# Kernel tuning notes

Measured on AMD Instinct MI355X. Metric: run time of the kernel, lower is better.

Reference implementation:

```python
import jax, jax.numpy as jnp
import numpy as np

EPS = 1e-5
ROPE_BASE = 10000.0
N_HEAD = 16


def rms_norm(x, eps=EPS):
    return x * jax.lax.rsqrt(jnp.mean(x * x, axis=-1, keepdims=True) + eps)


def rope(x):
    # x: [B, H, L, D]; non-standard interleaved variant from the source:
    # x_odd = x[..., 1::2], x_even = x[..., ::2]
    # y = interleave(y_odd, y_even)
    B, H, L, D = x.shape
    inv_freq = 1.0 / (ROPE_BASE ** (jnp.arange(0, D, 2, dtype=jnp.float32) / D))
    angles = jnp.arange(L, dtype=jnp.float32)[:, None] * inv_freq[None, :]  # [L, D/2]
    cos, sin = jnp.cos(angles), jnp.sin(angles)
    x_odd = x[..., 1::2].astype(jnp.float32)
    x_even = x[..., ::2].astype(jnp.float32)
    y_odd = x_odd * cos - x_even * sin
    y_even = x_odd * sin + x_even * cos
    y = jnp.stack([y_odd, y_even], axis=-1).reshape(B, H, L, D)
    return y.astype(x.dtype)


def setup_inputs() -> dict:
    key = jax.random.key(0)
    k1, k2, k3 = jax.random.split(key, 3)
    B, L, HID = 2, 2048, 2048
    in_std = 0.5 * HID ** (-0.5)
    bound = (3 ** 0.5) * in_std
    x = jax.random.normal(k1, (B, L, HID), dtype=jnp.float32)
    W_qkv = jax.random.uniform(k2, (3 * HID, HID), minval=-bound, maxval=bound, dtype=jnp.float32)
    # out_proj is zero-initialized in the source; use small random weights so the
    # output (and gradients) are non-trivial for correctness checking.
    W_out = jax.random.uniform(k3, (HID, HID), minval=-bound, maxval=bound, dtype=jnp.float32)
    return {"x": x, "W_qkv": W_qkv, "W_out": W_out}


def reference(x, W_qkv, W_out):
    B, L, HID = x.shape
    D = HID // N_HEAD
    qkv = jnp.einsum('blc,fc->blf', x, W_qkv)  # [B, L, 3*HID]
    q, k, v = jnp.split(qkv, 3, axis=-1)
    def heads(t):
        return t.reshape(B, L, N_HEAD, D).transpose(0, 2, 1, 3)  # [B,H,L,D]
    q, k, v = heads(q), heads(k), heads(v)
    q = rope(rms_norm(q))
    k = rope(rms_norm(k))
    scale = 1.0 / jnp.sqrt(jnp.asarray(D, dtype=jnp.float32))
    scores = jnp.einsum('bhqd,bhkd->bhqk', q, k) * scale
    causal = jnp.tril(jnp.ones((L, L), dtype=bool))
    scores = jnp.where(causal, scores, -jnp.inf)
    attn = jax.nn.softmax(scores, axis=-1)
    out = jnp.einsum('bhqk,bhkd->bhqd', attn, v)
    out = out.transpose(0, 2, 1, 3).reshape(B, L, HID)
    return jnp.einsum('blc,fc->blf', out, W_out)
```

## Files before the change

kernel.cpp:

```cpp
#include <hip/hip_runtime.h>
#include <stdint.h>
#include <math.h>

typedef unsigned short u16;
typedef unsigned int u32;
typedef __attribute__((ext_vector_type(8))) short bf16x8;
typedef __attribute__((ext_vector_type(4))) float f32x4;

#define SEQ 2048
#define HID 2048
#define NH  16
#define DH  128
#define NB  2

typedef __attribute__((address_space(1))) const u32 gu32;
typedef __attribute__((address_space(3))) u32 lu32;

__device__ __forceinline__ u16 f2bf(float f) {
  u32 u = __float_as_uint(f);
  return (u16)((u + 0x7fffu + ((u >> 16) & 1u)) >> 16);
}
__device__ __forceinline__ float bf2f(u16 h) { return __uint_as_float(((u32)h) << 16); }

__device__ __forceinline__ void gload_lds16(const void* g, void* l) {
  __builtin_amdgcn_global_load_lds((gu32*)g, (lu32*)l, 16, 0, 0);
}

__global__ __launch_bounds__(256) void k_cvt3(const float* __restrict__ s0, u16* __restrict__ d0, int n0,
                                              const float* __restrict__ s1, u16* __restrict__ d1, int n1,
                                              const float* __restrict__ s2, u16* __restrict__ d2, int n2) {
  int i = blockIdx.x * 256 + threadIdx.x;
  int stride = gridDim.x * 256;
  int total = n0 + n1 + n2;
  for (; i < total; i += stride) {
    const float* s; u16* d; int k = i;
    if (k < n0) { s = s0; d = d0; }
    else if (k < n0 + n1) { s = s1; d = d1; k -= n0; }
    else { s = s2; d = d2; k -= n0 + n1; }
    float4 v = ((const float4*)s)[k];
    ushort4 o;
    o.x = f2bf(v.x); o.y = f2bf(v.y); o.z = f2bf(v.z); o.w = f2bf(v.w);
    ((ushort4*)d)[k] = o;
  }
}

template<int EPI>
__global__ __launch_bounds__(512, 2)
void k_gemm4(const u16* __restrict__ A, const u16* __restrict__ Bm,
             float* __restrict__ Cf, u16* __restrict__ Qr, u16* __restrict__ Kr, u16* __restrict__ Vr,
             int N, int K, int NX) {
  __shared__ alignas(16) char sA0[16384];
  __shared__ alignas(16) char sA1[16384];
  __shared__ alignas(16) char sB0[32768];
  __shared__ alignas(16) char sB1[32768];
  const int tid = threadIdx.x;
  const int wid = tid >> 6, lane = tid & 63;
  const int l15 = lane & 15, l4 = lane >> 4;
  const int wm = wid >> 2, wn = wid & 3;
  const int nwg = gridDim.x, bid = blockIdx.x;
  const int wg = (bid & 7) * (nwg >> 3) + (bid >> 3);
  const int bx = wg % NX, by = wg / NX;
  const int m0 = by * 128, n0 = bx * 256;
  const char* Ab = (const char*)A;
  const char* Bb = (const char*)Bm;
  const size_t rs = (size_t)K * 2;

  int aoff[4][2], boff[4][2];
  #pragma unroll
  for (int mm = 0; mm < 4; ++mm)
    #pragma unroll
    for (int ks = 0; ks < 2; ++ks) {
      int row = wm * 64 + mm * 16 + l15;
      aoff[mm][ks] = row * 128 + ((ks * 64 + 16 * l4) ^ ((row & 7) << 4));
    }
  #pragma unroll
  for (int nn = 0; nn < 4; ++nn)
    #pragma unroll
    for (int ks = 0; ks < 2; ++ks) {
      int row = wn * 64 + nn * 16 + l15;
      boff[nn][ks] = row * 128 + ((ks * 64 + 16 * l4) ^ ((row & 7) << 4));
    }

  f32x4 acc[4][4];
  #pragma unroll
  for (int i = 0; i < 4; ++i)
    #pragma unroll
    for (int jx = 0; jx < 4; ++jx) acc[i][jx] = (f32x4){0.f, 0.f, 0.f, 0.f};
  bf16x8 areg[4][2], breg[4][2];

  auto STG1 = [&](const char* src, char* dst) {
    int o = tid * 16;
    int row = o >> 7, cb = o & 127;
    gload_lds16(src + (size_t)row * rs + (cb ^ ((row & 7) << 4)), dst + wid * 1024);
  };
  auto STG2 = [&](const char* src, char* dst) {
    #pragma unroll
    for (int jj = 0; jj < 2; ++jj) {
      int o = jj * 8192 + tid * 16;
      int row = o >> 7, cb = o & 127;
      gload_lds16(src + (size_t)row * rs + (cb ^ ((row & 7) << 4)), dst + jj * 8192 + wid * 1024);
    }
  };
  auto RD = [&](const char* sA, const char* sB) {
    #pragma unroll
    for (int mm = 0; mm < 4; ++mm)
      #pragma unroll
      for (int ks = 0; ks < 2; ++ks) areg[mm][ks] = *(const bf16x8*)(sA + aoff[mm][ks]);
    #pragma unroll
    for (int nn = 0; nn < 4; ++nn)
      #pragma unroll
      for (int ks = 0; ks < 2; ++ks) breg[nn][ks] = *(const bf16x8*)(sB + boff[nn][ks]);
  };
  auto MF = [&](int ks) {
    #pragma unroll
    for (int mm = 0; mm < 4; ++mm)
      #pragma unroll
      for (int nn = 0; nn < 4; ++nn)
        acc[mm][nn] = __builtin_amdgcn_mfma_f32_16x16x32_bf16(areg[mm][ks], breg[nn][ks], acc[mm][nn], 0, 0, 0);
  };

  const int NIT = K >> 7;
  STG2(Bb + (size_t)n0 * rs, sB0);
  STG2(Bb + (size_t)(n0 + 128) * rs, sB0 + 16384);
  STG1(Ab + (size_t)m0 * rs, sA0);
  STG1(Ab + (size_t)(m0 + 64) * rs, sA0 + 8192);
  STG2(Bb + (size_t)n0 * rs + 128, sB1);
  STG2(Bb + (size_t)(n0 + 128) * rs + 128, sB1 + 16384);
  STG1(Ab + (size_t)m0 * rs + 128, sA1);
  asm volatile("s_waitcnt vmcnt(5)" ::: "memory");
  __builtin_amdgcn_sched_barrier(0);
  __builtin_amdgcn_s_barrier();

  for (int j = 0; j < NIT; ++j) {
    const size_t k1 = (size_t)(2 * j + 1) * 128;
    const size_t k2 = (size_t)(2 * j + 2) * 128;
    const size_t k3 = (size_t)(2 * j + 3) * 128;
    const bool g2 = (j + 1 < NIT);
    RD(sA0, sB0);
    STG1(Ab + (size_t)(m0 + 64) * rs + k1, sA1 + 8192);
    __builtin_amdgcn_s_barrier();
    asm volatile("s_waitcnt lgkmcnt(0)" ::: "memory");
    __builtin_amdgcn_sched_barrier(0);
    __builtin_amdgcn_s_setprio(1); MF(0); __builtin_amdgcn_s_setprio(0);
    __builtin_amdgcn_s_barrier();
    if (g2) {
      STG2(Bb + (size_t)n0 * rs + k2, sB0);
      STG2(Bb + (size_t)(n0 + 128) * rs + k2, sB0 + 16384);
      STG1(Ab + (size_t)m0 * rs + k2, sA0);
    }
    __builtin_amdgcn_s_barrier();
    __builtin_amdgcn_s_setprio(1); MF(1); __builtin_amdgcn_s_setprio(0);
    if (g2) { asm volatile("s_waitcnt vmcnt(5)" ::: "memory"); }
    else    { asm volatile("s_waitcnt vmcnt(0)" ::: "memory"); }
    __builtin_amdgcn_sched_barrier(0);
    __builtin_amdgcn_s_barrier();
    RD(sA1, sB1);
    if (g2) STG1(Ab + (size_t)(m0 + 64) * rs + k2, sA0 + 8192);
    __builtin_amdgcn_s_barrier();
    asm volatile("s_waitcnt lgkmcnt(0)" ::: "memory");
    __builtin_amdgcn_sched_barrier(0);
    __builtin_amdgcn_s_setprio(1); MF(0); __builtin_amdgcn_s_setprio(0);
    __builtin_amdgcn_s_barrier();
    if (g2) {
      STG2(Bb + (size_t)n0 * rs + k3, sB1);
      STG2(Bb + (size_t)(n0 + 128) * rs + k3, sB1 + 16384);
      STG1(Ab + (size_t)m0 * rs + k3, sA1);
    }
    __builtin_amdgcn_s_barrier();
    __builtin_amdgcn_s_setprio(1); MF(1); __builtin_amdgcn_s_setprio(0);
    if (g2) { asm volatile("s_waitcnt vmcnt(5)" ::: "memory"); }
    else    { asm volatile("s_waitcnt vmcnt(0)" ::: "memory"); }
    __builtin_amdgcn_sched_barrier(0);
    __builtin_amdgcn_s_barrier();
  }

  #pragma unroll
  for (int mi = 0; mi < 4; ++mi) {
    #pragma unroll
    for (int ni = 0; ni < 4; ++ni) {
      #pragma unroll
      for (int jj = 0; jj < 4; ++jj) {
        int gm = m0 + wm * 64 + mi * 16 + l4 * 4 + jj;
        int gn = n0 + wn * 64 + ni * 16 + l15;
        float v = acc[mi][ni][jj];
        if (EPI == 0) {
          int b = gm >> 11, l = gm & 2047;
          int which = gn >> 11, hid = gn & 2047;
          int h = hid >> 7, d = hid & 127;
          u16* dst = (which == 0) ? Qr : ((which == 1) ? Kr : Vr);
          dst[((size_t)(b * NH + h) * SEQ + l) * DH + d] = f2bf(v);
        } else {
          Cf[(size_t)gm * N + gn] = v;
        }
      }
    }
  }
}

__global__ __launch_bounds__(256) void k_vtr(const u16* __restrict__ Vr, u16* __restrict__ Vt) {
  __shared__ u16 tile[64][72];
  const int k0 = blockIdx.x * 64, d0 = blockIdx.y * 64, bh = blockIdx.z;
  const u16* src = Vr + ((size_t)bh << 18);
  u16* dst = Vt + ((size_t)bh << 18);
  const int tid = threadIdx.x;
  #pragma unroll
  for (int it = 0; it < 2; ++it) {
    int e = it * 2048 + tid * 8;
    int r = e >> 6, c = e & 63;
    bf16x8 v = *(const bf16x8*)(src + (size_t)(k0 + r) * DH + d0 + c);
    *(bf16x8*)&tile[r][c] = v;
  }
  __syncthreads();
  #pragma unroll
  for (int it = 0; it < 2; ++it) {
    int e = it * 2048 + tid * 8;
    int rd = e >> 6, ck = e & 63;
    bf16x8 w;
    #pragma unroll
    for (int i = 0; i < 8; ++i) w[i] = (short)tile[ck + i][rd];
    *(bf16x8*)(dst + (size_t)(d0 + rd) * SEQ + k0 + ck) = w;
  }
}

__global__ __launch_bounds__(256) void k_nrope2(u16* __restrict__ Qr, u16* __restrict__ Kr, float mq) {
  u16* T = blockIdx.y ? Kr : Qr;
  const float mul = blockIdx.y ? 1.0f : mq;
  const int r = blockIdx.x * 4 + (threadIdx.x >> 6);
  const int lane = threadIdx.x & 63;
  u16* p = T + ((size_t)r << 7) + lane * 2;
  u32 pr = *(const u32*)p;
  float xe = bf2f((u16)(pr & 0xffffu));
  float xo = bf2f((u16)(pr >> 16));
  float ss = xe * xe + xo * xo;
  #pragma unroll
  for (int off = 1; off < 64; off <<= 1) ss += __shfl_xor(ss, off);
  float rinv = rsqrtf(ss * (1.f / 128.f) + 1e-5f);
  float e = xe * rinv, o = xo * rinv;
  int pos = r & (SEQ - 1);
  float freq = exp2f(-0.20762050593046014f * (float)lane);
  float ang = (float)pos * freq;
  float sn, cs;
  sincosf(ang, &sn, &cs);
  u32 outw = (u32)f2bf((o * cs - e * sn) * mul) | ((u32)f2bf((o * sn + e * cs) * mul) << 16);
  *(u32*)p = outw;
}

__device__ __forceinline__ void smax(f32x4 (&sacc)[4], float& m_, float& se,
                                     f32x4* accO, u32 (&pw)[8],
                                     bool diag, int qpos, int kb, int l15, int l4) {
  if (diag) {
    #pragma unroll
    for (int sj = 0; sj < 4; ++sj)
      #pragma unroll
      for (int j = 0; j < 4; ++j) {
        int kpos = kb + sj * 16 + l4 * 4 + j;
        if (kpos > qpos) sacc[sj][j] = -1e30f;
      }
  }
  float mx = sacc[0][0];
  #pragma unroll
  for (int sj = 0; sj < 4; ++sj)
    #pragma unroll
    for (int j = 0; j < 4; ++j) mx = fmaxf(mx, sacc[sj][j]);
  mx = fmaxf(mx, __shfl_xor(mx, 16));
  mx = fmaxf(mx, __shfl_xor(mx, 32));
  if (!__all(mx <= m_ + 8.f)) {
    float mn = fmaxf(m_, mx);
    float corr = __builtin_exp2f(m_ - mn);
    m_ = mn;
    se *= corr;
    float corr4[4];
    #pragma unroll
    for (int j = 0; j < 4; ++j) corr4[j] = __shfl(corr, l4 * 4 + j);
    #pragma unroll
    for (int db = 0; db < 8; ++db) {
      f32x4 a = accO[db];
      #pragma unroll
      for (int j = 0; j < 4; ++j) a[j] *= corr4[j];
      accO[db] = a;
    }
  }
  float sum = 0.f;
  #pragma unroll
  for (int sj = 0; sj < 4; ++sj)
    #pragma unroll
    for (int jp = 0; jp < 2; ++jp) {
      float p0 = __builtin_exp2f(sacc[sj][jp * 2]     - m_);
      float p1 = __builtin_exp2f(sacc[sj][jp * 2 + 1] - m_);
      pw[sj * 2 + jp] = (u32)f2bf(p0) | ((u32)f2bf(p1) << 16);
      sum += p0 + p1;
    }
  sum += __shfl_xor(sum, 16);
  sum += __shfl_xor(sum, 32);
  se += sum;
}

__device__ __forceinline__ void pwrite(char* sPw, const u32 (&pw)[8], int l15, int l4) {
  const int sw = (l15 & 7) << 4;
  char* base = sPw + l15 * 128;
  #pragma unroll
  for (int sj = 0; sj < 4; ++sj)
    #pragma unroll
    for (int jp = 0; jp < 2; ++jp)
      *(u32*)(base + ((sj * 32 + l4 * 8 + jp * 4) ^ sw)) = pw[sj * 2 + jp];
}

__device__ __forceinline__ void stage_kv(const char* Kp, const char* Vtp, int kb,
                                         char* bK, char* bV, int tid, int wid) {
  #pragma unroll
  for (int it = 0; it < 4; ++it) {
    int o = it * 4096 + tid * 16;
    int row = o >> 8, cb = o & 255;
    int scb = cb ^ ((row & 7) << 4);
    gload_lds16(Kp + (size_t)(kb + row) * 256 + scb, &bK[it * 4096 + wid * 1024]);
  }
  #pragma unroll
  for (int it = 0; it < 4; ++it) {
    int o = it * 4096 + tid * 16;
    int row = o >> 7, cb = o & 127;
    int scb = cb ^ ((row & 7) << 4);
    gload_lds16(Vtp + (size_t)row * (SEQ * 2) + kb * 2 + scb, &bV[it * 4096 + wid * 1024]);
  }
}

__global__ __launch_bounds__(256, 2)
void k_attn(const u16* __restrict__ Q, const u16* __restrict__ Kg,
            const u16* __restrict__ Vt, u16* __restrict__ O) {
  __shared__ alignas(16) char sK0[64 * 256];
  __shared__ alignas(16) char sK1[64 * 256];
  __shared__ alignas(16) char sV0[128 * 128];
  __shared__ alignas(16) char sV1[128 * 128];
  __shared__ alignas(16) char sP[4 * 2048];
  const int tid = threadIdx.x, wid = tid >> 6, lane = tid & 63;
  const int l15 = lane & 15, l4 = lane >> 4;
  const int i = blockIdx.x;
  const int xcd = i & 7, slot = i >> 3;
  const int p = slot & 15;
  const int bh = xcd + 8 * (slot >> 4);
  const int b = bh >> 4, h = bh & 15;
  const int tA = p, tB = 31 - p;
  const u16* Qp = Q + ((size_t)bh << 18);
  const char* Kp = (const char*)(Kg + ((size_t)bh << 18));
  const char* Vtp = (const char*)(Vt + ((size_t)bh << 18));
  const int q0A = tA * 64 + wid * 16;
  const int q0B = tB * 64 + wid * 16;

  bf16x8 aqA[4], aqB[4];
  #pragma unroll
  for (int kk = 0; kk < 4; ++kk) {
    aqA[kk] = *(const bf16x8*)(Qp + (size_t)(q0A + l15) * DH + kk * 32 + 8 * l4);
    aqB[kk] = *(const bf16x8*)(Qp + (size_t)(q0B + l15) * DH + kk * 32 + 8 * l4);
  }

  f32x4 accA[8], accB[8];
  #pragma unroll
  for (int i2 = 0; i2 < 8; ++i2) { accA[i2] = (f32x4){0.f,0.f,0.f,0.f}; accB[i2] = (f32x4){0.f,0.f,0.f,0.f}; }
  float mA = -1e30f, mB = -1e30f, seA = 0.f, seB = 0.f;

  char* sPw = sP + wid * 2048;
  const int psw = (l15 & 7) << 4;
  const int nt = tB + 1;

  stage_kv(Kp, Vtp, 0, sK0, sV0, tid, wid);
  for (int t = 0; t < nt; ++t) {
    char* bK = (t & 1) ? sK1 : sK0;
    char* bV = (t & 1) ? sV1 : sV0;
    if (t + 1 < nt) {
      stage_kv(Kp, Vtp, (t + 1) << 6, (t & 1) ? sK0 : sK1, (t & 1) ? sV0 : sV1, tid, wid);
      asm volatile("s_waitcnt vmcnt(8)" ::: "memory");
    } else {
      asm volatile("s_waitcnt vmcnt(0)" ::: "memory");
    }
    __builtin_amdgcn_sched_barrier(0);
    __builtin_amdgcn_s_barrier();

    const int kb = t << 6;
    if (t <= tA) {
      f32x4 sb[4], sa[4];
      __builtin_amdgcn_s_setprio(1);
      #pragma unroll
      for (int sj = 0; sj < 4; ++sj) {
        sb[sj] = (f32x4){0.f,0.f,0.f,0.f};
        sa[sj] = (f32x4){0.f,0.f,0.f,0.f};
        int row = sj * 16 + l15;
        const char* rK = bK + (row << 8);
        int swr = (row & 7) << 4;
        #pragma unroll
        for (int kk = 0; kk < 4; ++kk) {
          bf16x8 bkv = *(const bf16x8*)(rK + ((kk * 64 + 16 * l4) ^ swr));
          sb[sj] = __builtin_amdgcn_mfma_f32_16x16x32_bf16(bkv, aqB[kk], sb[sj], 0, 0, 0);
          sa[sj] = __builtin_amdgcn_mfma_f32_16x16x32_bf16(bkv, aqA[kk], sa[sj], 0, 0, 0);
        }
      }
      __builtin_amdgcn_s_setprio(0);
      u32 pwB[8], pwA[8];
      smax(sb, mB, seB, accB, pwB, false, 0, kb, l15, l4);
      smax(sa, mA, seA, accA, pwA, t == tA, q0A + l15, kb, l15, l4);
      pwrite(sPw, pwB, l15, l4);
      bf16x8 paB0 = *(const bf16x8*)(sPw + l15 * 128 + ((16 * l4) ^ psw));
      bf16x8 paB1 = *(const bf16x8*)(sPw + l15 * 128 + ((64 + 16 * l4) ^ psw));
      pwrite(sPw, pwA, l15, l4);
      bf16x8 paA0 = *(const bf16x8*)(sPw + l15 * 128 + ((16 * l4) ^ psw));
      bf16x8 paA1 = *(const bf16x8*)(sPw + l15 * 128 + ((64 + 16 * l4) ^ psw));
      __builtin_amdgcn_s_setprio(1);
      #pragma unroll
      for (int db = 0; db < 8; ++db) {
        int row = db * 16 + l15;
        const char* vb = bV + row * 128;
        int swr = (row & 7) << 4;
        bf16x8 b0 = *(const bf16x8*)(vb + ((16 * l4) ^ swr));
        bf16x8 b1 = *(const bf16x8*)(vb + ((64 + 16 * l4) ^ swr));
        accB[db] = __builtin_amdgcn_mfma_f32_16x16x32_bf16(paB0, b0, accB[db], 0, 0, 0);
        accA[db] = __builtin_amdgcn_mfma_f32_16x16x32_bf16(paA0, b0, accA[db], 0, 0, 0);
        accB[db] = __builtin_amdgcn_mfma_f32_16x16x32_bf16(paB1, b1, accB[db], 0, 0, 0);
        accA[db] = __builtin_amdgcn_mfma_f32_16x16x32_bf16(paA1, b1, accA[db], 0, 0, 0);
      }
      __builtin_amdgcn_s_setprio(0);
    } else {
      f32x4 sb[4];
      __builtin_amdgcn_s_setprio(1);
      #pragma unroll
      for (int sj = 0; sj < 4; ++sj) {
        sb[sj] = (f32x4){0.f,0.f,0.f,0.f};
        int row = sj * 16 + l15;
        const char* rK = bK + (row << 8);
        int swr = (row & 7) << 4;
        #pragma unroll
        for (int kk = 0; kk < 4; ++kk) {
          bf16x8 bkv = *(const bf16x8*)(rK + ((kk * 64 + 16 * l4) ^ swr));
          sb[sj] = __builtin_amdgcn_mfma_f32_16x16x32_bf16(bkv, aqB[kk], sb[sj], 0, 0, 0);
        }
      }
      __builtin_amdgcn_s_setprio(0);
      u32 pwB[8];
      smax(sb, mB, seB, accB, pwB, t == tB, q0B + l15, kb, l15, l4);
      pwrite(sPw, pwB, l15, l4);
      bf16x8 paB0 = *(const bf16x8*)(sPw + l15 * 128 + ((16 * l4) ^ psw));
      bf16x8 paB1 = *(const bf16x8*)(sPw + l15 * 128 + ((64 + 16 * l4) ^ psw));
      __builtin_amdgcn_s_setprio(1);
      #pragma unroll
      for (int db = 0; db < 8; ++db) {
        int row = db * 16 + l15;
        const char* vb = bV + row * 128;
        int swr = (row & 7) << 4;
        bf16x8 b0 = *(const bf16x8*)(vb + ((16 * l4) ^ swr));
        bf16x8 b1 = *(const bf16x8*)(vb + ((64 + 16 * l4) ^ swr));
        accB[db] = __builtin_amdgcn_mfma_f32_16x16x32_bf16(paB0, b0, accB[db], 0, 0, 0);
        accB[db] = __builtin_amdgcn_mfma_f32_16x16x32_bf16(paB1, b1, accB[db], 0, 0, 0);
      }
      __builtin_amdgcn_s_setprio(0);
    }

    __builtin_amdgcn_s_barrier();
  }

  float seA4[4], seB4[4];
  #pragma unroll
  for (int j = 0; j < 4; ++j) {
    seA4[j] = __shfl(seA, l4 * 4 + j);
    seB4[j] = __shfl(seB, l4 * 4 + j);
  }
  #pragma unroll
  for (int db = 0; db < 8; ++db) {
    #pragma unroll
    for (int j = 0; j < 4; ++j) {
      int d = db * 16 + l15;
      int qA = q0A + l4 * 4 + j;
      int qB = q0B + l4 * 4 + j;
      O[(size_t)(b * SEQ + qA) * HID + h * DH + d] = f2bf(accA[db][j] / seA4[j]);
      O[(size_t)(b * SEQ + qB) * HID + h * DH + d] = f2bf(accB[db][j] / seB4[j]);
    }
  }
}

extern "C" void kernel_launch(void* const* d_in, const int* in_sizes, int n_in,
                              void* d_out, int out_size, void* d_ws, size_t ws_size,
                              hipStream_t stream) {
  (void)in_sizes; (void)n_in; (void)out_size; (void)ws_size;
  const float* x = (const float*)d_in[0];
  const float* Wqkv = (const float*)d_in[1];
  const float* Wout = (const float*)d_in[2];
  float* out = (float*)d_out;
  char* ws = (char*)d_ws;

  u16* xb  = (u16*)(ws);
  u16* wqb = (u16*)(ws + (size_t)16777216);
  u16* Vt  = wqb;
  u16* wob = (u16*)(ws + (size_t)16777216 + 25165824);
  u16* Qr  = (u16*)(ws + (size_t)50331648);
  u16* Kr  = Qr + (size_t)8388608;
  u16* Vr  = Kr + (size_t)8388608;
  u16* Ob  = xb;

  const float mq = 0.08838834764831845f * 1.4426950408889634f;

  k_cvt3<<<dim3(2048), dim3(256), 0, stream>>>(x, xb, (NB * SEQ * HID) / 4,
                                               Wqkv, wqb, (3 * HID * HID) / 4,
                                               Wout, wob, (HID * HID) / 4);

  k_gemm4<0><<<dim3(768), dim3(512), 0, stream>>>(xb, wqb, nullptr, Qr, Kr, Vr, 3 * HID, HID, 24);

  k_vtr<<<dim3(SEQ / 64, DH / 64, NB * NH), dim3(256), 0, stream>>>(Vr, Vt);
  k_nrope2<<<dim3((NB * NH * SEQ) / 4, 2), dim3(256), 0, stream>>>(Qr, Kr, mq);

  k_attn<<<dim3(512), dim3(256), 0, stream>>>(Qr, Kr, Vt, Ob);

  k_gemm4<1><<<dim3(256), dim3(512), 0, stream>>>(Ob, wob, out, nullptr, nullptr, nullptr, HID, HID, 8);
}
```

Measured before the change: 311.3 us.

## Restructure attention to 256-query blocks and use simple 128x128 QKV GEMM

Attention now launches 256 blocks of 512 threads, each owning a contiguous 256-query slab with eight waves each handling 32 adjacent rows, instead of pairing a short and long 64-row tile to balance causal work. Per-wave activity and diagonal masking flags are computed per KV tile. The QKV projection switches from the double-buffered 512-thread GEMM to a new single-buffered 128x128 GEMM with 1536 blocks. The slab mapping gives blocks unequal causal work (4 to 32 KV tiles), and the new GEMM loses load/compute overlap, so both changes risk poorer utilisation.

```diff
diff --git a/kernel.cpp b/kernel.cpp
--- a/kernel.cpp
+++ b/kernel.cpp
@@ -41,6 +41,95 @@
     ushort4 o;
     o.x = f2bf(v.x); o.y = f2bf(v.y); o.z = f2bf(v.z); o.w = f2bf(v.w);
     ((ushort4*)d)[k] = o;
+  }
+}
+
+template<int EPI>
+__global__ __launch_bounds__(256)
+void k_gemm(const u16* __restrict__ A, const u16* __restrict__ Bm,
+            float* __restrict__ Cf, u16* __restrict__ Qr, u16* __restrict__ Kr, u16* __restrict__ Vr,
+            int N, int K, int NX) {
+  __shared__ alignas(16) char sA[128 * 128];
+  __shared__ alignas(16) char sB[128 * 128];
+  const int tid = threadIdx.x;
+  const int wid = tid >> 6, lane = tid & 63;
+  const int l15 = lane & 15, l4 = lane >> 4;
+  const int nwg = gridDim.x, bid = blockIdx.x;
+  const int wg = (bid & 7) * (nwg >> 3) + (bid >> 3);
+  const int bx = wg % NX, by = wg / NX;
+  const int m0 = by * 128, n0 = bx * 128;
+  const int wr = (wid >> 1) * 64, wc = (wid & 1) * 64;
+
+  f32x4 acc[4][4];
+  #pragma unroll
+  for (int i = 0; i < 4; ++i)
+    #pragma unroll
+    for (int j = 0; j < 4; ++j)
+      acc[i][j] = (f32x4){0.f, 0.f, 0.f, 0.f};
+
+  const int nkt = K >> 6;
+  for (int kt = 0; kt < nkt; ++kt) {
+    const int k0 = kt << 6;
+    __syncthreads();
+    #pragma unroll
+    for (int it = 0; it < 4; ++it) {
+      int o = it * 4096 + tid * 16;
+      int row = o >> 7, cb = o & 127;
+      int scb = cb ^ ((row & 7) << 4);
+      gload_lds16((const char*)A + ((size_t)(m0 + row) * K + k0) * 2 + scb, &sA[it * 4096 + wid * 1024]);
+    }
+    #pragma unroll
+    for (int it = 0; it < 4; ++it) {
+      int o = it * 4096 + tid * 16;
+      int row = o >> 7, cb = o & 127;
+      int scb = cb ^ ((row & 7) << 4);
+      gload_lds16((const char*)Bm + ((size_t)(n0 + row) * K + k0) * 2 + scb, &sB[it * 4096 + wid * 1024]);
+    }
+    __syncthreads();
+    #pragma unroll
+    for (int kk = 0; kk < 2; ++kk) {
+      bf16x8 av[4], bv[4];
+      #pragma unroll
+      for (int mi = 0; mi < 4; ++mi) {
+        int row = wr + mi * 16 + l15;
+        int colb = kk * 64 + 16 * l4;
+        av[mi] = *(const bf16x8*)&sA[row * 128 + (colb ^ ((row & 7) << 4))];
+      }
+      #pragma unroll
+      for (int ni = 0; ni < 4; ++ni) {
+        int row = wc + ni * 16 + l15;
+        int colb = kk * 64 + 16 * l4;
+        bv[ni] = *(const bf16x8*)&sB[row * 128 + (colb ^ ((row & 7) << 4))];
+      }
+      #pragma unroll
+      for (int mi = 0; mi < 4; ++mi)
+        #pragma unroll
+        for (int ni = 0; ni < 4; ++ni)
+          acc[mi][ni] = __builtin_amdgcn_mfma_f32_16x16x32_bf16(av[mi], bv[ni], acc[mi][ni], 0, 0, 0);
+    }
+  }
+
+  #pragma unroll
+  for (int mi = 0; mi < 4; ++mi) {
+    #pragma unroll
+    for (int ni = 0; ni < 4; ++ni) {
+      #pragma unroll
+      for (int j = 0; j < 4; ++j) {
+        int gm = m0 + wr + mi * 16 + l4 * 4 + j;
+        int gn = n0 + wc + ni * 16 + l15;
+        float v = acc[mi][ni][j];
+        if (EPI == 0) {
+          int b = gm >> 11, l = gm & 2047;
+          int which = gn >> 11, hid = gn & 2047;
+          int h = hid >> 7, d = hid & 127;
+          u16* dst = (which == 0) ? Qr : ((which == 1) ? Kr : Vr);
+          size_t idx = ((size_t)(b * NH + h) * SEQ + l) * DH + d;
+          dst[idx] = f2bf(v);
+        } else {
+          Cf[(size_t)gm * N + gn] = v;
+        }
+      }
+    }
   }
 }
 
@@ -305,69 +394,65 @@
       *(u32*)(base + ((sj * 32 + l4 * 8 + jp * 4) ^ sw)) = pw[sj * 2 + jp];
 }
 
-__device__ __forceinline__ void stage_kv(const char* Kp, const char* Vtp, int kb,
-                                         char* bK, char* bV, int tid, int wid) {
-  #pragma unroll
-  for (int it = 0; it < 4; ++it) {
-    int o = it * 4096 + tid * 16;
+__device__ __forceinline__ void stage_kv8(const char* Kp, const char* Vtp, int kb,
+                                          char* bK, char* bV, int tid, int wid) {
+  #pragma unroll
+  for (int it = 0; it < 2; ++it) {
+    int o = it * 8192 + tid * 16;
     int row = o >> 8, cb = o & 255;
-    int scb = cb ^ ((row & 7) << 4);
-    gload_lds16(Kp + (size_t)(kb + row) * 256 + scb, &bK[it * 4096 + wid * 1024]);
-  }
-  #pragma unroll
-  for (int it = 0; it < 4; ++it) {
-    int o = it * 4096 + tid * 16;
+    gload_lds16(Kp + (size_t)(kb + row) * 256 + (cb ^ ((row & 7) << 4)), bK + it * 8192 + wid * 1024);
+  }
+  #pragma unroll
+  for (int it = 0; it < 2; ++it) {
+    int o = it * 8192 + tid * 16;
     int row = o >> 7, cb = o & 127;
-    int scb = cb ^ ((row & 7) << 4);
-    gload_lds16(Vtp + (size_t)row * (SEQ * 2) + kb * 2 + scb, &bV[it * 4096 + wid * 1024]);
-  }
-}
-
-__global__ __launch_bounds__(256, 2)
+    gload_lds16(Vtp + (size_t)row * (SEQ * 2) + kb * 2 + (cb ^ ((row & 7) << 4)), bV + it * 8192 + wid * 1024);
+  }
+}
+
+__global__ __launch_bounds__(512, 1)
 void k_attn(const u16* __restrict__ Q, const u16* __restrict__ Kg,
             const u16* __restrict__ Vt, u16* __restrict__ O) {
-  __shared__ alignas(16) char sK0[64 * 256];
-  __shared__ alignas(16) char sK1[64 * 256];
-  __shared__ alignas(16) char sV0[128 * 128];
-  __shared__ alignas(16) char sV1[128 * 128];
-  __shared__ alignas(16) char sP[4 * 2048];
+  __shared__ alignas(16) char sK0[16384];
+  __shared__ alignas(16) char sK1[16384];
+  __shared__ alignas(16) char sV0[16384];
+  __shared__ alignas(16) char sV1[16384];
+  __shared__ alignas(16) char sP[8 * 2048];
   const int tid = threadIdx.x, wid = tid >> 6, lane = tid & 63;
   const int l15 = lane & 15, l4 = lane >> 4;
   const int i = blockIdx.x;
   const int xcd = i & 7, slot = i >> 3;
-  const int p = slot & 15;
-  const int bh = xcd + 8 * (slot >> 4);
+  const int bh = xcd + 8 * (slot >> 3);
+  const int s = slot & 7;
   const int b = bh >> 4, h = bh & 15;
-  const int tA = p, tB = 31 - p;
   const u16* Qp = Q + ((size_t)bh << 18);
   const char* Kp = (const char*)(Kg + ((size_t)bh << 18));
   const char* Vtp = (const char*)(Vt + ((size_t)bh << 18));
-  const int q0A = tA * 64 + wid * 16;
-  const int q0B = tB * 64 + wid * 16;
-
-  bf16x8 aqA[4], aqB[4];
+  const int q0w = s * 256 + wid * 32;
+
+  bf16x8 aq0[4], aq1[4];
   #pragma unroll
   for (int kk = 0; kk < 4; ++kk) {
-    aqA[kk] = *(const bf16x8*)(Qp + (size_t)(q0A + l15) * DH + kk * 32 + 8 * l4);
-    aqB[kk] = *(const bf16x8*)(Qp + (size_t)(q0B + l15) * DH + kk * 32 + 8 * l4);
-  }
-
-  f32x4 accA[8], accB[8];
-  #pragma unroll
-  for (int i2 = 0; i2 < 8; ++i2) { accA[i2] = (f32x4){0.f,0.f,0.f,0.f}; accB[i2] = (f32x4){0.f,0.f,0.f,0.f}; }
-  float mA = -1e30f, mB = -1e30f, seA = 0.f, seB = 0.f;
+    aq0[kk] = *(const bf16x8*)(Qp + (size_t)(q0w + l15) * DH + kk * 32 + 8 * l4);
+    aq1[kk] = *(const bf16x8*)(Qp + (size_t)(q0w + 16 + l15) * DH + kk * 32 + 8 * l4);
+  }
+
+  f32x4 acc0[8], acc1[8];
+  #pragma unroll
+  for (int i2 = 0; i2 < 8; ++i2) { acc0[i2] = (f32x4){0.f,0.f,0.f,0.f}; acc1[i2] = (f32x4){0.f,0.f,0.f,0.f}; }
+  float m0_ = -1e30f, m1_ = -1e30f, se0 = 0.f, se1 = 0.f;
 
   char* sPw = sP + wid * 2048;
   const int psw = (l15 & 7) << 4;
-  const int nt = tB + 1;
-
-  stage_kv(Kp, Vtp, 0, sK0, sV0, tid, wid);
+  const int nt = 4 * (s + 1);
+
+  stage_kv8(Kp, Vtp, 0, sK0, sV0, tid, wid);
   for (int t = 0; t < nt; ++t) {
     char* bK = (t & 1) ? sK1 : sK0;
     char* bV = (t & 1) ? sV1 : sV0;
     if (t + 1 < nt) {
-      stage_kv(Kp, Vtp, (t + 1) << 6, (t & 1) ? sK0 : sK1, (t & 1) ? sV0 : sV1, tid, wid);
-      asm volatile("s_waitcnt vmcnt(8)" ::: "memory");
+      stage_kv8(Kp, Vtp, (t + 1) << 6, (t & 1) ? sK0 : sK1, (t & 1) ? sV0 : sV1, tid, wid);
+      asm volatile("s_waitcnt vmcnt(4)" ::: "memory");
     } else {
       asm volatile("s_waitcnt vmcnt(0)" ::: "memory");
     }
@@ -375,33 +460,37 @@
     __builtin_amdgcn_s_barrier();
 
     const int kb = t << 6;
-    if (t <= tA) {
-      f32x4 sb[4], sa[4];
+    const bool act0 = (kb <= q0w + 15);
+    const bool act1 = (kb <= q0w + 31);
+    const bool dg0 = (kb + 63 > q0w);
+    const bool dg1 = (kb + 63 > q0w + 16);
+    if (act0) {
+      f32x4 s0v[4], s1v[4];
       __builtin_amdgcn_s_setprio(1);
       #pragma unroll
       for (int sj = 0; sj < 4; ++sj) {
-        sb[sj] = (f32x4){0.f,0.f,0.f,0.f};
-        sa[sj] = (f32x4){0.f,0.f,0.f,0.f};
+        s0v[sj] = (f32x4){0.f,0.f,0.f,0.f};
+        s1v[sj] = (f32x4){0.f,0.f,0.f,0.f};
         int row = sj * 16 + l15;
         const char* rK = bK + (row << 8);
         int swr = (row & 7) << 4;
         #pragma unroll
         for (int kk = 0; kk < 4; ++kk) {
           bf16x8 bkv = *(const bf16x8*)(rK + ((kk * 64 + 16 * l4) ^ swr));
-          sb[sj] = __builtin_amdgcn_mfma_f32_16x16x32_bf16(bkv, aqB[kk], sb[sj], 0, 0, 0);
-          sa[sj] = __builtin_amdgcn_mfma_f32_16x16x32_bf16(bkv, aqA[kk], sa[sj], 0, 0, 0);
+          s1v[sj] = __builtin_amdgcn_mfma_f32_16x16x32_bf16(bkv, aq1[kk], s1v[sj], 0, 0, 0);
+          s0v[sj] = __builtin_amdgcn_mfma_f32_16x16x32_bf16(bkv, aq0[kk], s0v[sj], 0, 0, 0);
         }
       }
       __builtin_amdgcn_s_setprio(0);
-      u32 pwB[8], pwA[8];
-      smax(sb, mB, seB, accB, pwB, false, 0, kb, l15, l4);
-      smax(sa, mA, seA, accA, pwA, t == tA, q0A + l15, kb, l15, l4);
-      pwrite(sPw, pwB, l15, l4);
-      bf16x8 paB0 = *(const bf16x8*)(sPw + l15 * 128 + ((16 * l4) ^ psw));
-      bf16x8 paB1 = *(const bf16x8*)(sPw + l15 * 128 + ((64 + 16 * l4) ^ psw));
-      pwrite(sPw, pwA, l15, l4);
-      bf16x8 paA0 = *(const bf16x8*)(sPw + l15 * 128 + ((16 * l4) ^ psw));
-      bf16x8 paA1 = *(const bf16x8*)(sPw + l15 * 128 + ((64 + 16 * l4) ^ psw));
+      u32 pw1[8], pw0[8];
+      smax(s1v, m1_, se1, acc1, pw1, dg1, q0w + 16 + l15, kb, l15, l4);
+      smax(s0v, m0_, se0, acc0, pw0, dg0, q0w + l15, kb, l15, l4);
+      pwrite(sPw, pw1, l15, l4);
+      bf16x8 pa10 = *(const bf16x8*)(sPw + l15 * 128 + ((16 * l4) ^ psw));
+      bf16x8 pa11 = *(const bf16x8*)(sPw + l15 * 128 + ((64 + 16 * l4) ^ psw));
+      pwrite(sPw, pw0, l15, l4);
+      bf16x8 pa00 = *(const bf16x8*)(sPw + l15 * 128 + ((16 * l4) ^ psw));
+      bf16x8 pa01 = *(const bf16x8*)(sPw + l15 * 128 + ((64 + 16 * l4) ^ psw));
       __builtin_amdgcn_s_setprio(1);
       #pragma unroll
       for (int db = 0; db < 8; ++db) {
@@ -410,33 +499,33 @@
         int swr = (row & 7) << 4;
         bf16x8 b0 = *(const bf16x8*)(vb + ((16 * l4) ^ swr));
         bf16x8 b1 = *(const bf16x8*)(vb + ((64 + 16 * l4) ^ swr));
-        accB[db] = __builtin_amdgcn_mfma_f32_16x16x32_bf16(paB0, b0, accB[db], 0, 0, 0);
-        accA[db] = __builtin_amdgcn_mfma_f32_16x16x32_bf16(paA0, b0, accA[db], 0, 0, 0);
-        accB[db] = __builtin_amdgcn_mfma_f32_16x16x32_bf16(paB1, b1, accB[db], 0, 0, 0);
-        accA[db] = __builtin_amdgcn_mfma_f32_16x16x32_bf16(paA1, b1, accA[db], 0, 0, 0);
+        acc1[db] = __builtin_amdgcn_mfma_f32_16x16x32_bf16(pa10, b0, acc1[db], 0, 0, 0);
+        acc0[db] = __builtin_amdgcn_mfma_f32_16x16x32_bf16(pa00, b0, acc0[db], 0, 0, 0);
+        acc1[db] = __builtin_amdgcn_mfma_f32_16x16x32_bf16(pa11, b1, acc1[db], 0, 0, 0);
+        acc0[db] = __builtin_amdgcn_mfma_f32_16x16x32_bf16(pa01, b1, acc0[db], 0, 0, 0);
       }
       __builtin_amdgcn_s_setprio(0);
-    } else {
-      f32x4 sb[4];
+    } else if (act1) {
+      f32x4 s1v[4];
       __builtin_amdgcn_s_setprio(1);
       #pragma unroll
       for (int sj = 0; sj < 4; ++sj) {
-        sb[sj] = (f32x4){0.f,0.f,0.f,0.f};
+        s1v[sj] = (f32x4){0.f,0.f,0.f,0.f};
         int row = sj * 16 + l15;
         const char* rK = bK + (row << 8);
         int swr = (row & 7) << 4;
         #pragma unroll
         for (int kk = 0; kk < 4; ++kk) {
           bf16x8 bkv = *(const bf16x8*)(rK + ((kk * 64 + 16 * l4) ^ swr));
-          sb[sj] = __builtin_amdgcn_mfma_f32_16x16x32_bf16(bkv, aqB[kk], sb[sj], 0, 0, 0);
+          s1v[sj] = __builtin_amdgcn_mfma_f32_16x16x32_bf16(bkv, aq1[kk], s1v[sj], 0, 0, 0);
         }
       }
       __builtin_amdgcn_s_setprio(0);
-      u32 pwB[8];
-      smax(sb, mB, seB, accB, pwB, t == tB, q0B + l15, kb, l15, l4);
-      pwrite(sPw, pwB, l15, l4);
-      bf16x8 paB0 = *(const bf16x8*)(sPw + l15 * 128 + ((16 * l4) ^ psw));
-      bf16x8 paB1 = *(const bf16x8*)(sPw + l15 * 128 + ((64 + 16 * l4) ^ psw));
+      u32 pw1[8];
+      smax(s1v, m1_, se1, acc1, pw1, dg1, q0w + 16 + l15, kb, l15, l4);
+      pwrite(sPw, pw1, l15, l4);
+      bf16x8 pa10 = *(const bf16x8*)(sPw + l15 * 128 + ((16 * l4) ^ psw));
+      bf16x8 pa11 = *(const bf16x8*)(sPw + l15 * 128 + ((64 + 16 * l4) ^ psw));
       __builtin_amdgcn_s_setprio(1);
       #pragma unroll
       for (int db = 0; db < 8; ++db) {
@@ -445,8 +534,8 @@
         int swr = (row & 7) << 4;
         bf16x8 b0 = *(const bf16x8*)(vb + ((16 * l4) ^ swr));
         bf16x8 b1 = *(const bf16x8*)(vb + ((64 + 16 * l4) ^ swr));
-        accB[db] = __builtin_amdgcn_mfma_f32_16x16x32_bf16(paB0, b0, accB[db], 0, 0, 0);
-        accB[db] = __builtin_amdgcn_mfma_f32_16x16x32_bf16(paB1, b1, accB[db], 0, 0, 0);
+        acc1[db] = __builtin_amdgcn_mfma_f32_16x16x32_bf16(pa10, b0, acc1[db], 0, 0, 0);
+        acc1[db] = __builtin_amdgcn_mfma_f32_16x16x32_bf16(pa11, b1, acc1[db], 0, 0, 0);
       }
       __builtin_amdgcn_s_setprio(0);
     }
@@ -454,21 +543,21 @@
     __builtin_amdgcn_s_barrier();
   }
 
-  float seA4[4], seB4[4];
+  float se04[4], se14[4];
   #pragma unroll
   for (int j = 0; j < 4; ++j) {
-    seA4[j] = __shfl(seA, l4 * 4 + j);
-    seB4[j] = __shfl(seB, l4 * 4 + j);
+    se04[j] = __shfl(se0, l4 * 4 + j);
+    se14[j] = __shfl(se1, l4 * 4 + j);
   }
   #pragma unroll
   for (int db = 0; db < 8; ++db) {
     #pragma unroll
     for (int j = 0; j < 4; ++j) {
       int d = db * 16 + l15;
-      int qA = q0A + l4 * 4 + j;
-      int qB = q0B + l4 * 4 + j;
-      O[(size_t)(b * SEQ + qA) * HID + h * DH + d] = f2bf(accA[db][j] / seA4[j]);
-      O[(size_t)(b * SEQ + qB) * HID + h * DH + d] = f2bf(accB[db][j] / seB4[j]);
+      int q0 = q0w + l4 * 4 + j;
+      int q1 = q0w + 16 + l4 * 4 + j;
+      O[(size_t)(b * SEQ + q0) * HID + h * DH + d] = f2bf(acc0[db][j] / se04[j]);
+      O[(size_t)(b * SEQ + q1) * HID + h * DH + d] = f2bf(acc1[db][j] / se14[j]);
     }
   }
 }
@@ -498,12 +587,12 @@
                                                Wqkv, wqb, (3 * HID * HID) / 4,
                                                Wout, wob, (HID * HID) / 4);
 
-  k_gemm4<0><<<dim3(768), dim3(512), 0, stream>>>(xb, wqb, nullptr, Qr, Kr, Vr, 3 * HID, HID, 24);
+  k_gemm<0><<<dim3(1536), dim3(256), 0, stream>>>(xb, wqb, nullptr, Qr, Kr, Vr, 3 * HID, HID, 48);
 
   k_vtr<<<dim3(SEQ / 64, DH / 64, NB * NH), dim3(256), 0, stream>>>(Vr, Vt);
   k_nrope2<<<dim3((NB * NH * SEQ) / 4, 2), dim3(256), 0, stream>>>(Qr, Kr, mq);
 
-  k_attn<<<dim3(512), dim3(256), 0, stream>>>(Qr, Kr, Vt, Ob);
+  k_attn<<<dim3(256), dim3(512), 0, stream>>>(Qr, Kr, Vt, Ob);
 
   k_gemm4<1><<<dim3(256), dim3(512), 0, stream>>>(Ob, wob, out, nullptr, nullptr, nullptr, HID, HID, 8);
 }
```

Result: slower. 326.5 us (+4.9%).

## Fuse V transpose into QKV GEMM epilogue with simpler 128x128 GEMM

Applied to the files above, without the earlier changes.

Replaces the heavily pipelined 128x256 double-buffered GEMM for the QKV projection with a new single-buffered 128x128 tile GEMM whose epilogue writes V directly in transposed [d, seq] layout. This removes the separate V transpose kernel and its extra global round-trip. The new GEMM has no LDS double buffering or prefetch overlap and does scalar strided stores for the transposed V, which may make the projection itself slower.

```diff
diff --git a/kernel.cpp b/kernel.cpp
--- a/kernel.cpp
+++ b/kernel.cpp
@@ -45,10 +45,102 @@
 }
 
 template<int EPI>
+__global__ __launch_bounds__(256)
+void k_gemm(const u16* __restrict__ A, const u16* __restrict__ Bm,
+            float* __restrict__ Cf, u16* __restrict__ Qr, u16* __restrict__ Kr, u16* __restrict__ Vt,
+            int N, int K, int NX) {
+  __shared__ alignas(16) char sA[128 * 128];
+  __shared__ alignas(16) char sB[128 * 128];
+  const int tid = threadIdx.x;
+  const int wid = tid >> 6, lane = tid & 63;
+  const int l15 = lane & 15, l4 = lane >> 4;
+  const int nwg = gridDim.x, bid = blockIdx.x;
+  const int wg = (bid & 7) * (nwg >> 3) + (bid >> 3);
+  const int bx = wg % NX, by = wg / NX;
+  const int m0 = by * 128, n0 = bx * 128;
+  const int wr = (wid >> 1) * 64, wc = (wid & 1) * 64;
+
+  f32x4 acc[4][4];
+  #pragma unroll
+  for (int i = 0; i < 4; ++i)
+    #pragma unroll
+    for (int j = 0; j < 4; ++j)
+      acc[i][j] = (f32x4){0.f, 0.f, 0.f, 0.f};
+
+  const int nkt = K >> 6;
+  for (int kt = 0; kt < nkt; ++kt) {
+    const int k0 = kt << 6;
+    __syncthreads();
+    #pragma unroll
+    for (int it = 0; it < 4; ++it) {
+      int o = it * 4096 + tid * 16;
+      int row = o >> 7, cb = o & 127;
+      int scb = cb ^ ((row & 7) << 4);
+      gload_lds16((const char*)A + ((size_t)(m0 + row) * K + k0) * 2 + scb, &sA[it * 4096 + wid * 1024]);
+    }
+    #pragma unroll
+    for (int it = 0; it < 4; ++it) {
+      int o = it * 4096 + tid * 16;
+      int row = o >> 7, cb = o & 127;
+      int scb = cb ^ ((row & 7) << 4);
+      gload_lds16((const char*)Bm + ((size_t)(n0 + row) * K + k0) * 2 + scb, &sB[it * 4096 + wid * 1024]);
+    }
+    __syncthreads();
+    #pragma unroll
+    for (int kk = 0; kk < 2; ++kk) {
+      bf16x8 av[4], bv[4];
+      #pragma unroll
+      for (int mi = 0; mi < 4; ++mi) {
+        int row = wr + mi * 16 + l15;
+        int colb = kk * 64 + 16 * l4;
+        av[mi] = *(const bf16x8*)&sA[row * 128 + (colb ^ ((row & 7) << 4))];
+      }
+      #pragma unroll
+      for (int ni = 0; ni < 4; ++ni) {
+        int row = wc + ni * 16 + l15;
+        int colb = kk * 64 + 16 * l4;
+        bv[ni] = *(const bf16x8*)&sB[row * 128 + (colb ^ ((row & 7) << 4))];
+      }
+      #pragma unroll
+      for (int mi = 0; mi < 4; ++mi)
+        #pragma unroll
+        for (int ni = 0; ni < 4; ++ni)
+          acc[mi][ni] = __builtin_amdgcn_mfma_f32_16x16x32_bf16(av[mi], bv[ni], acc[mi][ni], 0, 0, 0);
+    }
+  }
+
+  #pragma unroll
+  for (int mi = 0; mi < 4; ++mi) {
+    #pragma unroll
+    for (int ni = 0; ni < 4; ++ni) {
+      #pragma unroll
+      for (int j = 0; j < 4; ++j) {
+        int gm = m0 + wr + mi * 16 + l4 * 4 + j;
+        int gn = n0 + wc + ni * 16 + l15;
+        float v = acc[mi][ni][j];
+        if (EPI == 0) {
+          int b = gm >> 11, l = gm & 2047;
+          int which = gn >> 11, hid = gn & 2047;
+          int h = hid >> 7, d = hid & 127;
+          size_t bh18 = (size_t)(b * NH + h) << 18;
+          if (which == 2) {
+            Vt[bh18 + (size_t)d * SEQ + l] = f2bf(v);
+          } else {
+            u16* dst = (which == 0) ? Qr : Kr;
+            dst[bh18 + (size_t)l * DH + d] = f2bf(v);
+          }
+        } else {
+          Cf[(size_t)gm * N + gn] = v;
+        }
+      }
+    }
+  }
+}
+
+template<int EPI>
 __global__ __launch_bounds__(512, 2)
 void k_gemm4(const u16* __restrict__ A, const u16* __restrict__ Bm,
-             float* __restrict__ Cf, u16* __restrict__ Qr, u16* __restrict__ Kr, u16* __restrict__ Vr,
-             int N, int K, int NX) {
+             float* __restrict__ Cf, int N, int K, int NX) {
   __shared__ alignas(16) char sA0[16384];
   __shared__ alignas(16) char sA1[16384];
   __shared__ alignas(16) char sB0[32768];
@@ -182,43 +274,9 @@
       for (int jj = 0; jj < 4; ++jj) {
         int gm = m0 + wm * 64 + mi * 16 + l4 * 4 + jj;
         int gn = n0 + wn * 64 + ni * 16 + l15;
-        float v = acc[mi][ni][jj];
-        if (EPI == 0) {
-          int b = gm >> 11, l = gm & 2047;
-          int which = gn >> 11, hid = gn & 2047;
-          int h = hid >> 7, d = hid & 127;
-          u16* dst = (which == 0) ? Qr : ((which == 1) ? Kr : Vr);
-          dst[((size_t)(b * NH + h) * SEQ + l) * DH + d] = f2bf(v);
-        } else {
-          Cf[(size_t)gm * N + gn] = v;
-        }
-      }
-    }
-  }
-}
-
-__global__ __launch_bounds__(256) void k_vtr(const u16* __restrict__ Vr, u16* __restrict__ Vt) {
-  __shared__ u16 tile[64][72];
-  const int k0 = blockIdx.x * 64, d0 = blockIdx.y * 64, bh = blockIdx.z;
-  const u16* src = Vr + ((size_t)bh << 18);
-  u16* dst = Vt + ((size_t)bh << 18);
-  const int tid = threadIdx.x;
-  #pragma unroll
-  for (int it = 0; it < 2; ++it) {
-    int e = it * 2048 + tid * 8;
-    int r = e >> 6, c = e & 63;
-    bf16x8 v = *(const bf16x8*)(src + (size_t)(k0 + r) * DH + d0 + c);
-    *(bf16x8*)&tile[r][c] = v;
-  }
-  __syncthreads();
-  #pragma unroll
-  for (int it = 0; it < 2; ++it) {
-    int e = it * 2048 + tid * 8;
-    int rd = e >> 6, ck = e & 63;
-    bf16x8 w;
-    #pragma unroll
-    for (int i = 0; i < 8; ++i) w[i] = (short)tile[ck + i][rd];
-    *(bf16x8*)(dst + (size_t)(d0 + rd) * SEQ + k0 + ck) = w;
+        Cf[(size_t)gm * N + gn] = acc[mi][ni][jj];
+      }
+    }
   }
 }
 
@@ -485,11 +543,10 @@
 
   u16* xb  = (u16*)(ws);
   u16* wqb = (u16*)(ws + (size_t)16777216);
-  u16* Vt  = wqb;
   u16* wob = (u16*)(ws + (size_t)16777216 + 25165824);
   u16* Qr  = (u16*)(ws + (size_t)50331648);
   u16* Kr  = Qr + (size_t)8388608;
-  u16* Vr  = Kr + (size_t)8388608;
+  u16* Vt  = Kr + (size_t)8388608;
   u16* Ob  = xb;
 
   const float mq = 0.08838834764831845f * 1.4426950408889634f;
@@ -498,12 +555,11 @@
                                                Wqkv, wqb, (3 * HID * HID) / 4,
                                                Wout, wob, (HID * HID) / 4);
 
-  k_gemm4<0><<<dim3(768), dim3(512), 0, stream>>>(xb, wqb, nullptr, Qr, Kr, Vr, 3 * HID, HID, 24);
-
-  k_vtr<<<dim3(SEQ / 64, DH / 64, NB * NH), dim3(256), 0, stream>>>(Vr, Vt);
+  k_gemm<0><<<dim3(1536), dim3(256), 0, stream>>>(xb, wqb, nullptr, Qr, Kr, Vt, 3 * HID, HID, 48);
+
   k_nrope2<<<dim3((NB * NH * SEQ) / 4, 2), dim3(256), 0, stream>>>(Qr, Kr, mq);
 
   k_attn<<<dim3(512), dim3(256), 0, stream>>>(Qr, Kr, Vt, Ob);
 
-  k_gemm4<1><<<dim3(256), dim3(512), 0, stream>>>(Ob, wob, out, nullptr, nullptr, nullptr, HID, HID, 8);
-}
+  k_gemm4<1><<<dim3(256), dim3(512), 0, stream>>>(Ob, wob, out, HID, HID, 8);
+}
```

After: 307.6 us. Within noise of the previous version (-1.2%).
